# Performance work log

Measured on AMD Instinct MI355X. Metric: run time of the kernel, lower is better.

Reference implementation:

```python
import jax, jax.numpy as jnp
import numpy as np

N_NODES = 32768   # 32 graphs x 1024 points
B_GRAPHS = 32
RATIO = 16
C_IN = 64
HEADS = 4
NEG_SLOPE = 0.2


def setup_inputs() -> dict:
    key = jax.random.key(0)
    ks = jax.random.split(key, 8)
    H, C = HEADS, C_IN
    x = jax.random.normal(ks[0], (N_NODES, C_IN), dtype=jnp.float32)
    edge_index = jax.random.randint(ks[1], (2, 1000), 0, N_NODES)  # ignored by forward
    batch = jnp.repeat(jnp.arange(B_GRAPHS), N_NODES // B_GRAPHS)  # sorted graph ids
    xcent_base = jax.random.normal(ks[2], (RATIO, C_IN), dtype=jnp.float32)
    s = 1.0 / np.sqrt(C_IN)
    W_l = jax.random.normal(ks[3], (C_IN, H * C), dtype=jnp.float32) * s
    b_l = jnp.zeros((H * C,), dtype=jnp.float32)
    W_r = jax.random.normal(ks[4], (C_IN, H * C), dtype=jnp.float32) * s
    b_r = jnp.zeros((H * C,), dtype=jnp.float32)
    att = jax.random.normal(ks[5], (H, C), dtype=jnp.float32) * s
    bias = jnp.zeros((C,), dtype=jnp.float32)
    return {"x": x, "edge_index": edge_index, "batch": batch,
            "xcent_base": xcent_base, "W_l": W_l, "b_l": b_l,
            "W_r": W_r, "b_r": b_r, "att": att, "bias": bias,
            "ratio": RATIO, "batch_size": B_GRAPHS}


def reference(x, edge_index, batch, xcent_base, W_l, b_l, W_r, b_r, att, bias,
              ratio, batch_size):
    # GATv2Conv bipartite: (x_src, x_dst=tiled xcent_base), concat=False (mean over heads)
    H, C = att.shape
    N = x.shape[0]
    T = batch_size * ratio                       # number of target centroids
    # edge list: each source node -> all `ratio` centroids of its graph
    src = jnp.repeat(jnp.arange(N), ratio)       # [E]
    tgt = jnp.tile(jnp.arange(ratio), N) + jnp.repeat(batch, ratio) * ratio  # [E]
    x_dst = jnp.tile(xcent_base, (batch_size, 1))          # [T, C_in]
    x_l = (x @ W_l + b_l).reshape(N, H, C)                 # source transform
    x_r = (x_dst @ W_r + b_r).reshape(T, H, C)             # target transform
    z = x_l[src] + x_r[tgt]                                # [E, H, C]
    z = jnp.where(z >= 0, z, NEG_SLOPE * z)                # LeakyReLU(0.2)
    logit = jnp.einsum('ehc,hc->eh', z, att)               # [E, H]
    # segment softmax over edges sharing a target centroid
    m = jax.ops.segment_max(logit, tgt, num_segments=T)
    ex = jnp.exp(logit - m[tgt])
    den = jax.ops.segment_sum(ex, tgt, num_segments=T)
    alpha = ex / den[tgt]                                  # [E, H]
    out = jax.ops.segment_sum(x_l[src] * alpha[:, :, None], tgt, num_segments=T)
    xcent = out.mean(axis=1) + bias                        # [T, C] (concat=False)
    batchcent = jnp.repeat(jnp.arange(batch_size), ratio)  # [T]
    return xcent, batchcent
```

## Files before the change

### kernel.cpp

```cpp
#include <hip/hip_runtime.h>


typedef __attribute__((ext_vector_type(8))) short short8;
typedef __attribute__((ext_vector_type(4))) float f32x4;

#define NPG 1024
#define NT 512

static __device__ __forceinline__ unsigned short f2bf(float f) {
    unsigned int u = __float_as_uint(f);
    u += 0x7fffu + ((u >> 16) & 1u);
    return (unsigned short)(u >> 16);
}
static __device__ __forceinline__ float bf2f(unsigned short u) {
    return __uint_as_float(((unsigned int)u) << 16);
}
static __device__ __forceinline__ unsigned int cvt2(float a, float b) {
    unsigned int r;
    asm("v_cvt_pk_bf16_f32 %0, %1, %2" : "=v"(r) : "v"(a), "v"(b));
    return r;
}

__global__ __launch_bounds__(256, 2) void k1_fused(const float* __restrict__ x,
                                                   const float* __restrict__ W_l,
                                                   const float* __restrict__ W_r,
                                                   const float* __restrict__ b_l,
                                                   const float* __restrict__ b_r,
                                                   const float* __restrict__ xcb,
                                                   const float* __restrict__ att,
                                                   unsigned short* __restrict__ ws_pvh,
                                                   float* __restrict__ ws_denp) {
    __shared__ __align__(16) unsigned char smraw[(256 + 64) * 72 * 2];
    __shared__ __align__(16) float XR4[256][16];
    __shared__ float SS[64];
    unsigned short (*As)[72]  = (unsigned short (*)[72])smraw;
    unsigned short (*xlT)[72] = (unsigned short (*)[72])smraw;
    unsigned short (*exT)[72] = (unsigned short (*)[72])(smraw + 256 * 72 * 2);
    unsigned short (*XCB)[72] = exT;

    const int t = threadIdx.x;
    const int blk = blockIdx.x;
    const int n0 = blk * 64;

    {
        int n = t >> 2, q = (t & 3) * 16;
        const float* p = x + (size_t)(n0 + n) * 64 + q;
        float4 v0 = *(const float4*)p;
        float4 v1 = *(const float4*)(p + 4);
        float4 v2 = *(const float4*)(p + 8);
        float4 v3 = *(const float4*)(p + 12);
        uint4 a, b;
        a.x = cvt2(v0.x, v0.y); a.y = cvt2(v0.z, v0.w);
        a.z = cvt2(v1.x, v1.y); a.w = cvt2(v1.z, v1.w);
        b.x = cvt2(v2.x, v2.y); b.y = cvt2(v2.z, v2.w);
        b.z = cvt2(v3.x, v3.y); b.w = cvt2(v3.z, v3.w);
        *(uint4*)(&As[n][q])     = a;
        *(uint4*)(&As[n][q + 8]) = b;
        int rr = t >> 4, k4 = (t & 15) * 4;
        float4 cv = *(const float4*)(xcb + rr * 64 + k4);
        uint2 cw; cw.x = cvt2(cv.x, cv.y); cw.y = cvt2(cv.z, cv.w);
        *(uint2*)(&XCB[rr][k4]) = cw;
    }
    __syncthreads();

    const int l = t & 63;
    const int h = __builtin_amdgcn_readfirstlane(t >> 6);
    const int lm = l & 15, lq = l >> 4;
    const int lk = lq * 8;

    short8 af[4][2], bfr[4][2], brf[4][2];
#pragma unroll
    for (int nt = 0; nt < 4; ++nt)
#pragma unroll
        for (int ks = 0; ks < 2; ++ks) {
            const float* wl = W_l + (size_t)(ks * 32 + lk) * 256 + h * 64 + nt * 16 + lm;
            const float* wr = W_r + (size_t)(ks * 32 + lk) * 256 + h * 64 + nt * 16 + lm;
            uint4 pl, pr;
            pl.x = cvt2(wl[0 * 256], wl[1 * 256]); pl.y = cvt2(wl[2 * 256], wl[3 * 256]);
            pl.z = cvt2(wl[4 * 256], wl[5 * 256]); pl.w = cvt2(wl[6 * 256], wl[7 * 256]);
            pr.x = cvt2(wr[0 * 256], wr[1 * 256]); pr.y = cvt2(wr[2 * 256], wr[3 * 256]);
            pr.z = cvt2(wr[4 * 256], wr[5 * 256]); pr.w = cvt2(wr[6 * 256], wr[7 * 256]);
            bfr[nt][ks] = *(short8*)&pl;
            brf[nt][ks] = *(short8*)&pr;
        }
#pragma unroll
    for (int mt = 0; mt < 4; ++mt)
#pragma unroll
        for (int ks = 0; ks < 2; ++ks)
            af[mt][ks] = *(const short8*)(&As[mt * 16 + lm][ks * 32 + lk]);
    short8 axc[2];
#pragma unroll
    for (int ks = 0; ks < 2; ++ks)
        axc[ks] = *(const short8*)(&XCB[lm][ks * 32 + lk]);

    f32x4 acc[4][4], axr[4];
#pragma unroll
    for (int mt = 0; mt < 4; ++mt)
#pragma unroll
        for (int nt = 0; nt < 4; ++nt) { f32x4 z = {0.f,0.f,0.f,0.f}; acc[mt][nt] = z; }
#pragma unroll
    for (int nt = 0; nt < 4; ++nt) { f32x4 z = {0.f,0.f,0.f,0.f}; axr[nt] = z; }
#pragma unroll
    for (int mt = 0; mt < 4; ++mt)
#pragma unroll
        for (int nt = 0; nt < 4; ++nt)
#pragma unroll
            for (int ks = 0; ks < 2; ++ks)
                acc[mt][nt] = __builtin_amdgcn_mfma_f32_16x16x32_bf16(
                    af[mt][ks], bfr[nt][ks], acc[mt][nt], 0, 0, 0);
#pragma unroll
    for (int nt = 0; nt < 4; ++nt)
#pragma unroll
        for (int ks = 0; ks < 2; ++ks)
            axr[nt] = __builtin_amdgcn_mfma_f32_16x16x32_bf16(
                axc[ks], brf[nt][ks], axr[nt], 0, 0, 0);

    __syncthreads();

#pragma unroll
    for (int nt = 0; nt < 4; ++nt) {
        float bl = b_l[h * 64 + nt * 16 + lm];
#pragma unroll
        for (int mt = 0; mt < 4; ++mt) {
            unsigned int d0 = (unsigned int)f2bf(acc[mt][nt][0] + bl) |
                              ((unsigned int)f2bf(acc[mt][nt][1] + bl) << 16);
            unsigned int d1 = (unsigned int)f2bf(acc[mt][nt][2] + bl) |
                              ((unsigned int)f2bf(acc[mt][nt][3] + bl) << 16);
            *(uint2*)(&xlT[h * 64 + nt * 16 + lm][mt * 16 + lq * 4]) = make_uint2(d0, d1);
        }
    }
    {
        float brv[4], atw[4], pj[4];
#pragma unroll
        for (int nt = 0; nt < 4; ++nt) {
            brv[nt] = b_r[h * 64 + nt * 16 + lm];
            atw[nt] = att[h * 64 + nt * 16 + lm];
        }
#pragma unroll
        for (int j = 0; j < 4; ++j) pj[j] = 0.f;
#pragma unroll
        for (int nt = 0; nt < 4; ++nt) {
            float4 w;
            w.x = axr[nt][0] + brv[nt]; w.y = axr[nt][1] + brv[nt];
            w.z = axr[nt][2] + brv[nt]; w.w = axr[nt][3] + brv[nt];
            *(float4*)(&XR4[h * 64 + nt * 16 + lm][lq * 4]) = w;
            pj[0] = fmaf(w.x, atw[nt], pj[0]); pj[1] = fmaf(w.y, atw[nt], pj[1]);
            pj[2] = fmaf(w.z, atw[nt], pj[2]); pj[3] = fmaf(w.w, atw[nt], pj[3]);
        }
#pragma unroll
        for (int j = 0; j < 4; ++j) {
            pj[j] += __shfl_xor(pj[j], 1); pj[j] += __shfl_xor(pj[j], 2);
            pj[j] += __shfl_xor(pj[j], 4); pj[j] += __shfl_xor(pj[j], 8);
        }
        if (lm == 0) {
#pragma unroll
            for (int j = 0; j < 4; ++j) SS[h * 16 + lq * 4 + j] = 0.6f * pj[j];
        }
    }
    __syncthreads();

    float base = 0.f;
    float lacc[16];
#pragma unroll
    for (int r = 0; r < 16; ++r) lacc[r] = 0.f;
#pragma unroll 4
    for (int c = 0; c < 64; ++c) {
        int row = h * 64 + c;
        float xv = bf2f(xlT[row][l]);
        float attv = att[row];
        base = fmaf(xv, attv, base);
        float a4 = 0.4f * attv;
        float xr4v[16];
        const float4* xp = (const float4*)(&XR4[row][0]);
        *(float4*)(xr4v + 0)  = xp[0];
        *(float4*)(xr4v + 4)  = xp[1];
        *(float4*)(xr4v + 8)  = xp[2];
        *(float4*)(xr4v + 12) = xp[3];
#pragma unroll
        for (int r = 0; r < 16; ++r)
            lacc[r] = fmaf(fabsf(xv + xr4v[r]), a4, lacc[r]);
    }
    base *= 0.6f;
#pragma unroll
    for (int r = 0; r < 16; ++r) {
        float ex = __expf(base + lacc[r] + SS[h * 16 + r]);
        exT[h * 16 + r][l] = f2bf(ex);
    }
    __syncthreads();

    short8 ap[2];
#pragma unroll
    for (int ks = 0; ks < 2; ++ks)
        ap[ks] = *(const short8*)(&exT[h * 16 + lm][ks * 32 + lk]);
    short o = (lm == 0) ? (short)0x3F80 : (short)0;
    short8 onesf = {o, o, o, o, o, o, o, o};

    f32x4 pacc[4], dacc;
    { f32x4 z = {0.f,0.f,0.f,0.f}; pacc[0]=z; pacc[1]=z; pacc[2]=z; pacc[3]=z; dacc=z; }
#pragma unroll
    for (int ks = 0; ks < 2; ++ks) {
#pragma unroll
        for (int nt = 0; nt < 4; ++nt) {
            short8 bp = *(const short8*)(&xlT[h * 64 + nt * 16 + lm][ks * 32 + lk]);
            pacc[nt] = __builtin_amdgcn_mfma_f32_16x16x32_bf16(ap[ks], bp, pacc[nt], 0, 0, 0);
        }
        dacc = __builtin_amdgcn_mfma_f32_16x16x32_bf16(ap[ks], onesf, dacc, 0, 0, 0);
    }

    unsigned short* pvb = ws_pvh + ((size_t)blk * 4 + h) * 1024;
#pragma unroll
    for (int nt = 0; nt < 4; ++nt)
#pragma unroll
        for (int j = 0; j < 4; ++j)
            pvb[(lq * 4 + j) * 64 + nt * 16 + lm] = f2bf(pacc[nt][j]);
    if (lm == 0) {
#pragma unroll
        for (int j = 0; j < 4; ++j)
            ws_denp[((size_t)blk * 4 + h) * 16 + lq * 4 + j] = dacc[j];
    }
}

__global__ __launch_bounds__(256) void k2_final(const unsigned short* __restrict__ ws_pvh,
                                                const float* __restrict__ ws_denp,
                                                const float* __restrict__ bias,
                                                float* __restrict__ out) {
    __shared__ float sm[4][64];
    int b = blockIdx.x;
    if (b < 512) {
        int g = b >> 4, r = b & 15;
        int c = threadIdx.x & 63, hw = threadIdx.x >> 6;
        float num = 0.f, den = 0.f;
#pragma unroll
        for (int tl = 0; tl < 16; ++tl) {
            num += bf2f(ws_pvh[(((size_t)(g * 16 + tl) * 4 + hw) * 16 + r) * 64 + c]);
            den += ws_denp[((size_t)(g * 16 + tl) * 4 + hw) * 16 + r];
        }
        sm[hw][c] = num / den;
        __syncthreads();
        if (threadIdx.x < 64) {
            float s = (sm[0][c] + sm[1][c]) + (sm[2][c] + sm[3][c]);
            out[(size_t)(g * 16 + r) * 64 + c] = fmaf(0.25f, s, bias[c]);
        }
    } else {
        int tt = (b - 512) * 256 + threadIdx.x;
        out[NT * 64 + tt] = (float)(tt >> 4);
    }
}

extern "C" void kernel_launch(void* const* d_in, const int* in_sizes, int n_in,
                              void* d_out, int out_size, void* d_ws, size_t ws_size,
                              hipStream_t stream) {
    const float* x    = (const float*)d_in[0];
    const float* xcb  = (const float*)d_in[3];
    const float* W_l  = (const float*)d_in[4];
    const float* b_l  = (const float*)d_in[5];
    const float* W_r  = (const float*)d_in[6];
    const float* b_r  = (const float*)d_in[7];
    const float* att  = (const float*)d_in[8];
    const float* bias = (const float*)d_in[9];
    float* out = (float*)d_out;

    unsigned short* ws_pvh = (unsigned short*)d_ws;
    float* ws_denp = (float*)(ws_pvh + 2097152);

    k1_fused<<<512, 256, 0, stream>>>(x, W_l, W_r, b_l, b_r, xcb, att, ws_pvh, ws_denp);
    k2_final<<<514, 256, 0, stream>>>(ws_pvh, ws_denp, bias, out);
}
```

Baseline: 26.34 us.

## Swizzle unpadded LDS tiles and store target transform as bf16

Replaces the padded 72-column shared-memory tiles with an unpadded 64-column buffer that uses an XOR swizzle on 8-element units to avoid bank conflicts. It also stores the per-centroid target transform XR4 as packed bf16 instead of fp32, halving its LDS footprint and read traffic in the logit loop. Together these cut LDS usage, which could help occupancy. The cost is extra index arithmetic and bf16 rounding of x_r in the attention logits, which lowers accuracy.

```diff
diff --git a/kernel.cpp b/kernel.cpp
--- a/kernel.cpp
+++ b/kernel.cpp
@@ -20,6 +20,7 @@
     asm("v_cvt_pk_bf16_f32 %0, %1, %2" : "=v"(r) : "v"(a), "v"(b));
     return r;
 }
+static __device__ __forceinline__ int swz(int row, int unit) { return (unit ^ (row & 7)) << 3; }
 
 __global__ __launch_bounds__(256, 2) void k1_fused(const float* __restrict__ x,
                                                    const float* __restrict__ W_l,
@@ -30,21 +31,17 @@
                                                    const float* __restrict__ att,
                                                    unsigned short* __restrict__ ws_pvh,
                                                    float* __restrict__ ws_denp) {
-    __shared__ __align__(16) unsigned char smraw[(256 + 64) * 72 * 2];
-    __shared__ __align__(16) float XR4[256][16];
+    __shared__ __align__(16) short LL[320][64];
+    __shared__ __align__(16) unsigned int XR4b[256][8];
     __shared__ float SS[64];
-    unsigned short (*As)[72]  = (unsigned short (*)[72])smraw;
-    unsigned short (*xlT)[72] = (unsigned short (*)[72])smraw;
-    unsigned short (*exT)[72] = (unsigned short (*)[72])(smraw + 256 * 72 * 2);
-    unsigned short (*XCB)[72] = exT;
 
     const int t = threadIdx.x;
     const int blk = blockIdx.x;
     const int n0 = blk * 64;
 
     {
-        int n = t >> 2, q = (t & 3) * 16;
-        const float* p = x + (size_t)(n0 + n) * 64 + q;
+        int n = t >> 2, u0 = (t & 3) * 2;
+        const float* p = x + (size_t)(n0 + n) * 64 + u0 * 8;
         float4 v0 = *(const float4*)p;
         float4 v1 = *(const float4*)(p + 4);
         float4 v2 = *(const float4*)(p + 8);
@@ -54,12 +51,12 @@
         a.z = cvt2(v1.x, v1.y); a.w = cvt2(v1.z, v1.w);
         b.x = cvt2(v2.x, v2.y); b.y = cvt2(v2.z, v2.w);
         b.z = cvt2(v3.x, v3.y); b.w = cvt2(v3.z, v3.w);
-        *(uint4*)(&As[n][q])     = a;
-        *(uint4*)(&As[n][q + 8]) = b;
-        int rr = t >> 4, k4 = (t & 15) * 4;
-        float4 cv = *(const float4*)(xcb + rr * 64 + k4);
+        *(uint4*)(&LL[n][swz(n, u0)])     = a;
+        *(uint4*)(&LL[n][swz(n, u0 + 1)]) = b;
+        int rr = 256 + (t >> 4), k4 = (t & 15) * 4;
+        float4 cv = *(const float4*)(xcb + (t >> 4) * 64 + k4);
         uint2 cw; cw.x = cvt2(cv.x, cv.y); cw.y = cvt2(cv.z, cv.w);
-        *(uint2*)(&XCB[rr][k4]) = cw;
+        *(uint2*)(&LL[rr][swz(rr, k4 >> 3) + (k4 & 7)]) = cw;
     }
     __syncthreads();
 
@@ -86,12 +83,16 @@
 #pragma unroll
     for (int mt = 0; mt < 4; ++mt)
 #pragma unroll
-        for (int ks = 0; ks < 2; ++ks)
-            af[mt][ks] = *(const short8*)(&As[mt * 16 + lm][ks * 32 + lk]);
+        for (int ks = 0; ks < 2; ++ks) {
+            int row = mt * 16 + lm;
+            af[mt][ks] = *(const short8*)(&LL[row][swz(row, ks * 4 + lq)]);
+        }
     short8 axc[2];
 #pragma unroll
-    for (int ks = 0; ks < 2; ++ks)
-        axc[ks] = *(const short8*)(&XCB[lm][ks * 32 + lk]);
+    for (int ks = 0; ks < 2; ++ks) {
+        int row = 256 + lm;
+        axc[ks] = *(const short8*)(&LL[row][swz(row, ks * 4 + lq)]);
+    }
 
     f32x4 acc[4][4], axr[4];
 #pragma unroll
@@ -126,7 +127,9 @@
                               ((unsigned int)f2bf(acc[mt][nt][1] + bl) << 16);
             unsigned int d1 = (unsigned int)f2bf(acc[mt][nt][2] + bl) |
                               ((unsigned int)f2bf(acc[mt][nt][3] + bl) << 16);
-            *(uint2*)(&xlT[h * 64 + nt * 16 + lm][mt * 16 + lq * 4]) = make_uint2(d0, d1);
+            int row = h * 64 + nt * 16 + lm;
+            int ncol = mt * 16 + lq * 4;
+            *(uint2*)(&LL[row][swz(row, ncol >> 3) + (ncol & 7)]) = make_uint2(d0, d1);
         }
     }
     {
@@ -143,7 +146,9 @@
             float4 w;
             w.x = axr[nt][0] + brv[nt]; w.y = axr[nt][1] + brv[nt];
             w.z = axr[nt][2] + brv[nt]; w.w = axr[nt][3] + brv[nt];
-            *(float4*)(&XR4[h * 64 + nt * 16 + lm][lq * 4]) = w;
+            unsigned int p0 = (unsigned int)f2bf(w.x) | ((unsigned int)f2bf(w.y) << 16);
+            unsigned int p1 = (unsigned int)f2bf(w.z) | ((unsigned int)f2bf(w.w) << 16);
+            *(uint2*)(&XR4b[h * 64 + nt * 16 + lm][lq * 2]) = make_uint2(p0, p1);
             pj[0] = fmaf(w.x, atw[nt], pj[0]); pj[1] = fmaf(w.y, atw[nt], pj[1]);
             pj[2] = fmaf(w.z, atw[nt], pj[2]); pj[3] = fmaf(w.w, atw[nt], pj[3]);
         }
@@ -166,16 +171,21 @@
 #pragma unroll 4
     for (int c = 0; c < 64; ++c) {
         int row = h * 64 + c;
-        float xv = bf2f(xlT[row][l]);
+        float xv = bf2f((unsigned short)LL[row][swz(row, l >> 3) + (l & 7)]);
         float attv = att[row];
         base = fmaf(xv, attv, base);
         float a4 = 0.4f * attv;
+        const uint4* xp = (const uint4*)(&XR4b[row][0]);
+        uint4 w0 = xp[0], w1 = xp[1];
         float xr4v[16];
-        const float4* xp = (const float4*)(&XR4[row][0]);
-        *(float4*)(xr4v + 0)  = xp[0];
-        *(float4*)(xr4v + 4)  = xp[1];
-        *(float4*)(xr4v + 8)  = xp[2];
-        *(float4*)(xr4v + 12) = xp[3];
+        xr4v[0]  = __uint_as_float(w0.x << 16); xr4v[1]  = __uint_as_float(w0.x & 0xffff0000u);
+        xr4v[2]  = __uint_as_float(w0.y << 16); xr4v[3]  = __uint_as_float(w0.y & 0xffff0000u);
+        xr4v[4]  = __uint_as_float(w0.z << 16); xr4v[5]  = __uint_as_float(w0.z & 0xffff0000u);
+        xr4v[6]  = __uint_as_float(w0.w << 16); xr4v[7]  = __uint_as_float(w0.w & 0xffff0000u);
+        xr4v[8]  = __uint_as_float(w1.x << 16); xr4v[9]  = __uint_as_float(w1.x & 0xffff0000u);
+        xr4v[10] = __uint_as_float(w1.y << 16); xr4v[11] = __uint_as_float(w1.y & 0xffff0000u);
+        xr4v[12] = __uint_as_float(w1.z << 16); xr4v[13] = __uint_as_float(w1.z & 0xffff0000u);
+        xr4v[14] = __uint_as_float(w1.w << 16); xr4v[15] = __uint_as_float(w1.w & 0xffff0000u);
 #pragma unroll
         for (int r = 0; r < 16; ++r)
             lacc[r] = fmaf(fabsf(xv + xr4v[r]), a4, lacc[r]);
@@ -184,14 +194,17 @@
 #pragma unroll
     for (int r = 0; r < 16; ++r) {
         float ex = __expf(base + lacc[r] + SS[h * 16 + r]);
-        exT[h * 16 + r][l] = f2bf(ex);
+        int row = 256 + h * 16 + r;
+        LL[row][swz(row, l >> 3) + (l & 7)] = (short)f2bf(ex);
     }
     __syncthreads();
 
     short8 ap[2];
 #pragma unroll
-    for (int ks = 0; ks < 2; ++ks)
-        ap[ks] = *(const short8*)(&exT[h * 16 + lm][ks * 32 + lk]);
+    for (int ks = 0; ks < 2; ++ks) {
+        int row = 256 + h * 16 + lm;
+        ap[ks] = *(const short8*)(&LL[row][swz(row, ks * 4 + lq)]);
+    }
     short o = (lm == 0) ? (short)0x3F80 : (short)0;
     short8 onesf = {o, o, o, o, o, o, o, o};
 
@@ -201,7 +214,8 @@
     for (int ks = 0; ks < 2; ++ks) {
 #pragma unroll
         for (int nt = 0; nt < 4; ++nt) {
-            short8 bp = *(const short8*)(&xlT[h * 64 + nt * 16 + lm][ks * 32 + lk]);
+            int row = h * 64 + nt * 16 + lm;
+            short8 bp = *(const short8*)(&LL[row][swz(row, ks * 4 + lq)]);
             pacc[nt] = __builtin_amdgcn_mfma_f32_16x16x32_bf16(ap[ks], bp, pacc[nt], 0, 0, 0);
         }
         dacc = __builtin_amdgcn_mfma_f32_16x16x32_bf16(ap[ks], onesf, dacc, 0, 0, 0);
```

After: 29.21 us. +10.9%, slower.
